# Kernel tuning notes

Hardware: AMD Instinct MI355X
Metric: run time of the kernel (lower is better)

Reference implementation:

```python
import jax, jax.numpy as jnp
import numpy as np

B = 2097152  # batch
H = 9        # hidden width
N_MID = 19   # fc2..fc20


def setup_inputs() -> dict:
    key = jax.random.key(0)
    ks = jax.random.split(key, 8)
    x = jax.random.normal(ks[0], (B, 2), dtype=jnp.float32)
    # PyTorch Linear init: U(-1/sqrt(fan_in), 1/sqrt(fan_in))
    def lin(k, out_f, in_f):
        kw, kb = jax.random.split(k)
        bound = 1.0 / np.sqrt(in_f)
        W = jax.random.uniform(kw, (out_f, in_f), jnp.float32, -bound, bound)
        b = jax.random.uniform(kb, (out_f,), jnp.float32, -bound, bound)
        return W, b
    W1, b1 = lin(ks[1], H, 2)
    # stacked middle layers fc2..fc20: [19, 9, 9] / [19, 9]
    kmids = jax.random.split(ks[2], N_MID)
    Wmid = jnp.stack([lin(k, H, H)[0] for k in kmids])
    bmid = jnp.stack([lin(jax.random.fold_in(k, 1), H, H)[1] for k in kmids])
    W21, b21 = lin(ks[3], 2, H)
    return {"x": x, "W1": W1, "b1": b1, "Wmid": Wmid, "bmid": bmid,
            "W21": W21, "b21": b21}


def reference(x, W1, b1, Wmid, bmid, W21, b21):
    h = jax.nn.elu(x @ W1.T + b1)  # [B, 9]
    def layer(h, wb):
        W, b = wb
        return jax.nn.elu(h @ W.T + b), None
    h, _ = jax.lax.scan(layer, h, (Wmid, bmid))
    logits = h @ W21.T + b21  # [B, 2]
    return jax.nn.log_softmax(logits, axis=1)
```

## Files before the change

kernel.cpp:

```cpp
#include <hip/hip_runtime.h>


typedef _Float16 half8 __attribute__((ext_vector_type(8)));
typedef _Float16 h2 __attribute__((ext_vector_type(2)));
typedef float float4v __attribute__((ext_vector_type(4)));
typedef unsigned int uint4v __attribute__((ext_vector_type(4)));

constexpr int H   = 9;
constexpr int NL  = 21;
constexpr int TPW = 8;
constexpr int BLK = 64;

__global__ void build_frags(const float* __restrict__ W1, const float* __restrict__ b1,
                            const float* __restrict__ Wmid, const float* __restrict__ bmid,
                            const float* __restrict__ W21, const float* __restrict__ b21,
                            _Float16* __restrict__ ws) {
    const float L   = 1.4426950408889634f;
    const float LN2 = 0.6931471805599453f;
    int l    = blockIdx.x;
    int lane = threadIdx.x;
    int row  = lane & 15;
    int g    = lane >> 4;
    bool orow = ((row & 3) != 3) && (row < 12);
    int  o    = row - (row >> 2);
    for (int j = 0; j < 8; ++j) {
        int k = g * 8 + j;
        float v = 0.0f;
        if (l == 0) {
            if (orow && k < 2)        v = L * W1[o * 2 + k];
            else if (orow && k == 24) v = L * b1[o];
        } else if (l <= 19) {
            const float* W = Wmid + (l - 1) * 81;
            const float* b = bmid + (l - 1) * 9;
            if (orow) {
                if (j < 3 && g < 3) {
                    int r_in = g * 4 + j;
                    int i = r_in - (r_in >> 2);
                    v = W[o * 9 + i];
                } else if (j >= 4 && j < 7 && g < 3) {
                    int r_in = g * 4 + (j - 4);
                    int i = r_in - (r_in >> 2);
                    v = L * W[o * 9 + i];
                } else if (k == 24) {
                    float s = 0.0f;
                    for (int i = 0; i < H; ++i) s += W[o * 9 + i];
                    v = L * (b[o] - s);
                }
            }
        } else {
            if (row < 2) {
                if (j < 3 && g < 3) {
                    int r_in = g * 4 + j;
                    int i = r_in - (r_in >> 2);
                    v = LN2 * W21[row * 9 + i];
                } else if (j >= 4 && j < 7 && g < 3) {
                    int r_in = g * 4 + (j - 4);
                    int i = r_in - (r_in >> 2);
                    v = W21[row * 9 + i];
                } else if (k == 24) {
                    float s = 0.0f;
                    for (int i = 0; i < H; ++i) s += W21[row * 9 + i];
                    v = b21[row] - s;
                }
            }
        }
        ws[l * 512 + lane * 8 + j] = (_Float16)v;
    }
}

__device__ __forceinline__ half8 act_to_b(float4v d, unsigned bias_or) {
    const h2 Z = {(_Float16)0.f, (_Float16)0.f};
    h2 p01 = __builtin_bit_cast(h2, __builtin_amdgcn_cvt_pkrtz(d[0], d[1]));
    h2 p2x = __builtin_bit_cast(h2, __builtin_amdgcn_cvt_pkrtz(d[2], 0.f));
    h2 r01 = __builtin_elementwise_max(p01, Z);
    h2 r2x = __builtin_elementwise_max(p2x, Z);
    float t0 = fminf(d[0], 0.f);
    float t1 = fminf(d[1], 0.f);
    float t2 = fminf(d[2], 0.f);
    float e0 = __builtin_amdgcn_exp2f(t0);
    float e1 = __builtin_amdgcn_exp2f(t1);
    float e2 = __builtin_amdgcn_exp2f(t2);
    uint4v u;
    u[0] = __builtin_bit_cast(unsigned, r01) | bias_or;
    u[1] = __builtin_bit_cast(unsigned, r2x);
    u[2] = __builtin_bit_cast(unsigned, __builtin_amdgcn_cvt_pkrtz(e0, e1));
    u[3] = __builtin_bit_cast(unsigned, __builtin_amdgcn_cvt_pkrtz(e2, 1.f));
    return __builtin_bit_cast(half8, u);
}

__device__ __forceinline__ half8 x_to_b(float2 xv, unsigned g0_sel, unsigned bias_or) {
    unsigned ux = __builtin_bit_cast(unsigned, __builtin_amdgcn_cvt_pkrtz(xv.x, xv.y));
    uint4v u;
    u[0] = (ux & g0_sel) | bias_or;
    u[1] = 0u; u[2] = 0u; u[3] = 0u;
    return __builtin_bit_cast(half8, u);
}

__device__ __forceinline__ float bperm(int byte_idx, float v) {
    return __builtin_bit_cast(float,
        __builtin_amdgcn_ds_bpermute(byte_idx, __builtin_bit_cast(int, v)));
}

__device__ __forceinline__ void run_group(const half8* __restrict__ A,
                                          const float2* __restrict__ xv,
                                          int gbase, int lane, int grp,
                                          unsigned g0_sel, unsigned bias_or,
                                          float* __restrict__ out) {
    const float4v ZV = {0.f, 0.f, 0.f, 0.f};
    const float NLOG2E = -1.4426950408889634f;
    const float LN2f   = 0.6931471805599453f;
    const int col = lane & 15;

    half8 bf[4];
    #pragma unroll
    for (int k = 0; k < 4; ++k) bf[k] = x_to_b(xv[k], g0_sel, bias_or);

    float4v dd[4];
    #pragma unroll
    for (int l = 0; l < NL; ++l) {
        #pragma unroll
        for (int k = 0; k < 4; ++k)
            dd[k] = __builtin_amdgcn_mfma_f32_16x16x32_f16(A[l], bf[k], ZV, 0, 0, 0);
        if (l < NL - 1) {
            #pragma unroll
            for (int k = 0; k < 4; ++k)
                bf[k] = act_to_b(dd[k], bias_or);
        }
    }

    const int bidx = col << 2;
    float a0 = bperm(bidx, dd[0][0]), a1 = bperm(bidx, dd[0][1]);
    float b0 = bperm(bidx, dd[1][0]), b1 = bperm(bidx, dd[1][1]);
    float c0 = bperm(bidx, dd[2][0]), c1 = bperm(bidx, dd[2][1]);
    float d0 = bperm(bidx, dd[3][0]), d1 = bperm(bidx, dd[3][1]);
    float l0 = (grp == 0) ? a0 : (grp == 1) ? b0 : (grp == 2) ? c0 : d0;
    float l1 = (grp == 0) ? a1 : (grp == 1) ? b1 : (grp == 2) ? c1 : d1;

    float mx  = fmaxf(l0, l1);
    float ad  = fabsf(l0 - l1);
    float e   = __builtin_amdgcn_exp2f(NLOG2E * ad);
    float lg  = __builtin_amdgcn_logf(1.0f + e);
    float lse = fmaf(LN2f, lg, mx);
    ((float2*)out)[(gbase << 4) + lane] = make_float2(l0 - lse, l1 - lse);
}

__global__ __launch_bounds__(BLK, 4) void mlp_mfma(const float* __restrict__ x,
                                                   const _Float16* __restrict__ ws,
                                                   float* __restrict__ out) {
    const int lane  = threadIdx.x;
    const int grp   = lane >> 4;
    const int col   = lane & 15;
    const int tile0 = blockIdx.x * TPW;

    half8 A[NL];
    const half8* wsv = (const half8*)ws;
    #pragma unroll
    for (int l = 0; l < NL; ++l) A[l] = wsv[l * 64 + lane];

    float2 xv[TPW];
    #pragma unroll
    for (int k = 0; k < TPW; ++k)
        xv[k] = ((const float2*)x)[((tile0 + k) << 4) + col];

    const unsigned bias_or = (grp == 3) ? 0x00003C00u : 0u;
    const unsigned g0_sel  = (grp == 0) ? 0xFFFFFFFFu : 0u;

    run_group(A, xv,     tile0,     lane, grp, g0_sel, bias_or, out);
    run_group(A, xv + 4, tile0 + 4, lane, grp, g0_sel, bias_or, out);
}

extern "C" void kernel_launch(void* const* d_in, const int* in_sizes, int n_in,
                              void* d_out, int out_size, void* d_ws, size_t ws_size,
                              hipStream_t stream) {
    const float* x    = (const float*)d_in[0];
    const float* W1   = (const float*)d_in[1];
    const float* b1   = (const float*)d_in[2];
    const float* Wmid = (const float*)d_in[3];
    const float* bmid = (const float*)d_in[4];
    const float* W21  = (const float*)d_in[5];
    const float* b21  = (const float*)d_in[6];
    float* out = (float*)d_out;
    _Float16* ws = (_Float16*)d_ws;

    build_frags<<<NL, 64, 0, stream>>>(W1, b1, Wmid, bmid, W21, b21, ws);

    const int nrows = in_sizes[0] / 2;
    const int tiles = nrows / 16;
    const int blocks = tiles / TPW;
    mlp_mfma<<<blocks, BLK, 0, stream>>>(x, ws, out);
}
```

Measured before the change: 176.9 us.

## Compute ELU exp in packed fp16 and interleave all eight tiles per layer

The ELU negative branch now clamps and exponentiates in packed fp16 rather than fp32, so each activation needs fewer transcendental and conversion instructions. The kernel also runs all eight tiles through each layer together instead of two sequential groups of four. Weight fragments are loaded per layer from global memory instead of being held in registers for all 21 layers, trading register pressure for repeated loads. This gives more independent MFMAs per layer to hide latency, at the cost of reduced exp precision and more live accumulators.

```diff
diff --git a/kernel.cpp b/kernel.cpp
--- a/kernel.cpp
+++ b/kernel.cpp
@@ -5,6 +5,8 @@
 typedef _Float16 h2 __attribute__((ext_vector_type(2)));
 typedef float float4v __attribute__((ext_vector_type(4)));
 typedef unsigned int uint4v __attribute__((ext_vector_type(4)));
+
+extern "C" __device__ _Float16 __ocml_exp2_f16(_Float16);
 
 constexpr int H   = 9;
 constexpr int NL  = 21;
@@ -74,17 +76,16 @@
     h2 p2x = __builtin_bit_cast(h2, __builtin_amdgcn_cvt_pkrtz(d[2], 0.f));
     h2 r01 = __builtin_elementwise_max(p01, Z);
     h2 r2x = __builtin_elementwise_max(p2x, Z);
-    float t0 = fminf(d[0], 0.f);
-    float t1 = fminf(d[1], 0.f);
-    float t2 = fminf(d[2], 0.f);
-    float e0 = __builtin_amdgcn_exp2f(t0);
-    float e1 = __builtin_amdgcn_exp2f(t1);
-    float e2 = __builtin_amdgcn_exp2f(t2);
+    h2 t01 = __builtin_elementwise_min(p01, Z);
+    h2 t2x = __builtin_elementwise_min(p2x, Z);
+    h2 e01 = __builtin_elementwise_exp2(t01);
+    _Float16 e2 = __ocml_exp2_f16(t2x[0]);
     uint4v u;
     u[0] = __builtin_bit_cast(unsigned, r01) | bias_or;
     u[1] = __builtin_bit_cast(unsigned, r2x);
-    u[2] = __builtin_bit_cast(unsigned, __builtin_amdgcn_cvt_pkrtz(e0, e1));
-    u[3] = __builtin_bit_cast(unsigned, __builtin_amdgcn_cvt_pkrtz(e2, 1.f));
+    u[2] = __builtin_bit_cast(unsigned, e01);
+    u[3] = 0x3C000000u |
+           (unsigned)__builtin_bit_cast(unsigned short, e2);
     return __builtin_bit_cast(half8, u);
 }
 
@@ -101,41 +102,18 @@
         __builtin_amdgcn_ds_bpermute(byte_idx, __builtin_bit_cast(int, v)));
 }
 
-__device__ __forceinline__ void run_group(const half8* __restrict__ A,
-                                          const float2* __restrict__ xv,
-                                          int gbase, int lane, int grp,
-                                          unsigned g0_sel, unsigned bias_or,
-                                          float* __restrict__ out) {
-    const float4v ZV = {0.f, 0.f, 0.f, 0.f};
+__device__ __forceinline__ void softmax4(const float4v* dd, int gbase,
+                                         int lane, int grp,
+                                         float* __restrict__ out) {
     const float NLOG2E = -1.4426950408889634f;
     const float LN2f   = 0.6931471805599453f;
-    const int col = lane & 15;
-
-    half8 bf[4];
-    #pragma unroll
-    for (int k = 0; k < 4; ++k) bf[k] = x_to_b(xv[k], g0_sel, bias_or);
-
-    float4v dd[4];
-    #pragma unroll
-    for (int l = 0; l < NL; ++l) {
-        #pragma unroll
-        for (int k = 0; k < 4; ++k)
-            dd[k] = __builtin_amdgcn_mfma_f32_16x16x32_f16(A[l], bf[k], ZV, 0, 0, 0);
-        if (l < NL - 1) {
-            #pragma unroll
-            for (int k = 0; k < 4; ++k)
-                bf[k] = act_to_b(dd[k], bias_or);
-        }
-    }
-
-    const int bidx = col << 2;
+    const int bidx = (lane & 15) << 2;
     float a0 = bperm(bidx, dd[0][0]), a1 = bperm(bidx, dd[0][1]);
     float b0 = bperm(bidx, dd[1][0]), b1 = bperm(bidx, dd[1][1]);
     float c0 = bperm(bidx, dd[2][0]), c1 = bperm(bidx, dd[2][1]);
     float d0 = bperm(bidx, dd[3][0]), d1 = bperm(bidx, dd[3][1]);
     float l0 = (grp == 0) ? a0 : (grp == 1) ? b0 : (grp == 2) ? c0 : d0;
     float l1 = (grp == 0) ? a1 : (grp == 1) ? b1 : (grp == 2) ? c1 : d1;
-
     float mx  = fmaxf(l0, l1);
     float ad  = fabsf(l0 - l1);
     float e   = __builtin_amdgcn_exp2f(NLOG2E * ad);
@@ -152,21 +130,36 @@
     const int col   = lane & 15;
     const int tile0 = blockIdx.x * TPW;
 
-    half8 A[NL];
     const half8* wsv = (const half8*)ws;
-    #pragma unroll
-    for (int l = 0; l < NL; ++l) A[l] = wsv[l * 64 + lane];
+    const unsigned bias_or = (grp == 3) ? 0x00003C00u : 0u;
+    const unsigned g0_sel  = (grp == 0) ? 0xFFFFFFFFu : 0u;
+    const float4v ZV = {0.f, 0.f, 0.f, 0.f};
 
     float2 xv[TPW];
     #pragma unroll
     for (int k = 0; k < TPW; ++k)
         xv[k] = ((const float2*)x)[((tile0 + k) << 4) + col];
 
-    const unsigned bias_or = (grp == 3) ? 0x00003C00u : 0u;
-    const unsigned g0_sel  = (grp == 0) ? 0xFFFFFFFFu : 0u;
+    half8 bf[TPW];
+    #pragma unroll
+    for (int k = 0; k < TPW; ++k) bf[k] = x_to_b(xv[k], g0_sel, bias_or);
 
-    run_group(A, xv,     tile0,     lane, grp, g0_sel, bias_or, out);
-    run_group(A, xv + 4, tile0 + 4, lane, grp, g0_sel, bias_or, out);
+    float4v dd[TPW];
+    #pragma unroll
+    for (int l = 0; l < NL; ++l) {
+        half8 A = wsv[l * 64 + lane];
+        #pragma unroll
+        for (int k = 0; k < TPW; ++k)
+            dd[k] = __builtin_amdgcn_mfma_f32_16x16x32_f16(A, bf[k], ZV, 0, 0, 0);
+        if (l < NL - 1) {
+            #pragma unroll
+            for (int k = 0; k < TPW; ++k)
+                bf[k] = act_to_b(dd[k], bias_or);
+        }
+    }
+
+    softmax4(dd,     tile0,     lane, grp, out);
+    softmax4(dd + 4, tile0 + 4, lane, grp, out);
 }
 
 extern "C" void kernel_launch(void* const* d_in, const int* in_sizes, int n_in,
```

Result: faster. 158.3 us (-10.5%).
